# Kernel optimization log

Measured on AMD Instinct MI355X. Metric: run time of the kernel, lower is better.

The kernel has to match this reference:

```python
import jax, jax.numpy as jnp
import numpy as np

B, S, DIM = 128, 256, 512          # batch, grid tokens (16*16), input feature dim
D = 128                             # embedding_dim
K = 16384                           # num_embeddings
GH = GW = 16                        # grid size
EPS = 1e-12


def setup_inputs() -> dict:
    key = jax.random.key(0)
    ks = jax.random.split(key, 10)
    return {
        "input_data_first": jax.random.normal(ks[0], (B, S, DIM), jnp.float32),
        "input_data_last": jax.random.normal(ks[1], (B, S, DIM), jnp.float32),
        "random_vector": jax.random.normal(ks[2], (B * 64, D), jnp.float32),
        "codebooks": jax.random.normal(ks[3], (K, D), jnp.float32),
        "W_in": jax.random.normal(ks[4], (DIM, D), jnp.float32) / np.sqrt(DIM),
        "b_in": jnp.zeros((D,), jnp.float32),
        "conv_w": jax.random.normal(ks[5], (D, D, 3, 3), jnp.float32) / np.sqrt(D * 9),
        "conv_b": jnp.zeros((D,), jnp.float32),
        "W_out": jax.random.normal(ks[6], (D, DIM), jnp.float32) / np.sqrt(D),
        "b_out": jnp.zeros((DIM,), jnp.float32),
        "codebooks_used": jnp.zeros((K,), jnp.int32),
    }


def _encode(x, W_in, b_in, conv_w, conv_b):
    h = x @ W_in + b_in                                  # [B,S,D]
    h = jnp.transpose(h, (0, 2, 1)).reshape(B, D, GH, GW)  # [B,D,16,16]
    h = jax.lax.conv_general_dilated(
        h, conv_w, window_strides=(2, 2), padding=[(1, 1), (1, 1)],
        dimension_numbers=("NCHW", "OIHW", "NCHW"))
    h = h + conv_b[None, :, None, None]                  # [B,D,8,8]
    h = h.reshape(B, D, -1)                              # [B,D,64]
    h = jnp.transpose(h, (0, 2, 1)).reshape(-1, D)       # [B*64, D]
    return h


def reference(input_data_first, input_data_last, random_vector, codebooks,
              W_in, b_in, conv_w, conv_b, W_out, b_out, codebooks_used):
    e_first = _encode(input_data_first, W_in, b_in, conv_w, conv_b)
    e_last = _encode(input_data_last, W_in, b_in, conv_w, conv_b)
    x = e_last - e_first                                 # [N,D]

    # squared-distance to every codebook entry: [N,K]
    dists = (jnp.sum(x * x, axis=1, keepdims=True)
             - 2.0 * (x @ codebooks.T)
             + jnp.sum(codebooks * codebooks, axis=1)[None, :])
    min_indices = jnp.argmin(dists, axis=1)              # [N]
    hard_q = codebooks[min_indices]                      # [N,D]

    norm_res = jnp.sqrt(jnp.sum((x - hard_q) ** 2, axis=1, keepdims=True))
    norm_rnd = jnp.sqrt(jnp.sum(random_vector ** 2, axis=1, keepdims=True))
    vq_error = (norm_res / norm_rnd + EPS) * random_vector
    quantized = x + vq_error                             # [N,D]

    counts = jnp.zeros((K,), jnp.float32).at[min_indices].add(1.0)
    avg_probs = counts / x.shape[0]
    perplexity = jnp.exp(-jnp.sum(avg_probs * jnp.log(avg_probs + EPS)))

    new_used = codebooks_used + counts.astype(jnp.int32)

    # decode (faithful to torch: raw memory reinterpretation, not inverse transpose)
    q = quantized.reshape(B, D, -1)                      # [B,D,64]
    q = jnp.transpose(q, (0, 2, 1))                      # [B,64,D]
    out = q @ W_out + b_out                              # [B,64,DIM]
    return out, perplexity, new_used, min_indices.reshape(B, -1)
```

## Files before the change

### kernel.cpp

```cpp
#include <hip/hip_runtime.h>
#include <math.h>

#define NROWS 8192
#define KCB   16384

using frag_ab = __attribute__((ext_vector_type(8))) short;
using frag_cd = __attribute__((ext_vector_type(4))) float;
using f32x4   = __attribute__((ext_vector_type(4))) float;

__device__ inline unsigned short f2bf(float f) {
    unsigned u = __float_as_uint(f);
    return (unsigned short)((u + 0x7FFFu + ((u >> 16) & 1u)) >> 16);
}

__global__ __launch_bounds__(256) void k_wt(const float* __restrict__ cw,
                                            float* __restrict__ W2) {
    int gid = blockIdx.x * 256 + threadIdx.x;
    if (gid >= 147456) return;
    int co = gid & 127;
    int ci = (gid >> 7) & 127;
    int kk = gid >> 14;
    W2[gid] = cw[(size_t)co * 1152 + ci * 9 + kk];
}

__global__ __launch_bounds__(256) void k_c2(const float* __restrict__ cb,
                                            float* __restrict__ c2f) {
    int k = blockIdx.x * 256 + threadIdx.x;
    const float* row = cb + (size_t)k * 128;
    double s = 0.0;
    #pragma unroll
    for (int d = 0; d < 128; d += 4) {
        float4 v = *(const float4*)(row + d);
        s += (double)v.x * v.x + (double)v.y * v.y
           + (double)v.z * v.z + (double)v.w * v.w;
    }
    c2f[k] = (float)s + 1024.0f;
}

__global__ __launch_bounds__(256) void k_cbbf(const float* __restrict__ cb,
                                              unsigned short* __restrict__ Cbb) {
    int gid = blockIdx.x * 256 + threadIdx.x;
    float4 v = ((const float4*)cb)[gid];
    ushort4 o;
    o.x = f2bf(v.x); o.y = f2bf(v.y); o.z = f2bf(v.z); o.w = f2bf(v.w);
    ((ushort4*)Cbb)[gid] = o;
}

__global__ __launch_bounds__(256) void k_encode_gemm(
    const float* __restrict__ last, const float* __restrict__ first,
    const float* __restrict__ W_in, double* __restrict__ H)
{
    __shared__ double As[32][64];
    __shared__ float  Bs[32][128];
    const int tid  = threadIdx.x;
    const int row0 = blockIdx.x * 64;
    const int tx = tid & 31;
    const int ty = tid >> 5;

    double acc[8][4];
    #pragma unroll
    for (int r = 0; r < 8; ++r)
        #pragma unroll
        for (int j = 0; j < 4; ++j) acc[r][j] = 0.0;

    for (int d0 = 0; d0 < 512; d0 += 32) {
        #pragma unroll
        for (int it = 0; it < 2; ++it) {
            int flat = it * 1024 + tid * 4;
            int r = flat >> 5, d = flat & 31;
            const float4 l4 = *(const float4*)(last  + (size_t)(row0 + r) * 512 + d0 + d);
            const float4 f4 = *(const float4*)(first + (size_t)(row0 + r) * 512 + d0 + d);
            As[d + 0][r] = (double)l4.x - (double)f4.x;
            As[d + 1][r] = (double)l4.y - (double)f4.y;
            As[d + 2][r] = (double)l4.z - (double)f4.z;
            As[d + 3][r] = (double)l4.w - (double)f4.w;
        }
        #pragma unroll
        for (int it = 0; it < 4; ++it) {
            int flat = it * 1024 + tid * 4;
            int d = flat >> 7, c = flat & 127;
            *(float4*)&Bs[d][c] = *(const float4*)(W_in + (size_t)(d0 + d) * 128 + c);
        }
        __syncthreads();
        #pragma unroll 4
        for (int d = 0; d < 32; ++d) {
            double a[8];
            #pragma unroll
            for (int q = 0; q < 4; ++q) {
                double2 t = *(const double2*)&As[d][ty * 8 + 2 * q];
                a[2 * q] = t.x; a[2 * q + 1] = t.y;
            }
            float4 bf = *(const float4*)&Bs[d][tx * 4];
            double b[4] = {(double)bf.x, (double)bf.y, (double)bf.z, (double)bf.w};
            #pragma unroll
            for (int r = 0; r < 8; ++r)
                #pragma unroll
                for (int j = 0; j < 4; ++j)
                    acc[r][j] = fma(a[r], b[j], acc[r][j]);
        }
        __syncthreads();
    }
    #pragma unroll
    for (int r = 0; r < 8; ++r) {
        double* o = H + (size_t)(row0 + ty * 8 + r) * 128 + tx * 4;
        o[0] = acc[r][0]; o[1] = acc[r][1]; o[2] = acc[r][2]; o[3] = acc[r][3];
    }
}

__global__ __launch_bounds__(256) void k_conv(
    const double* __restrict__ H, const float* __restrict__ W2,
    double* __restrict__ X, unsigned short* __restrict__ Xb)
{
    __shared__ double Hs[3 * 16 * 128];
    const int b   = blockIdx.x >> 3;
    const int oh  = blockIdx.x & 7;
    const int tid = threadIdx.x;
    const int ih0 = 2 * oh - 1;
    for (int it = 0; it < 24; ++it) {
        int idx = it * 256 + tid;
        int r = idx >> 11;
        int rem = idx & 2047;
        int ih = ih0 + r;
        Hs[idx] = (ih >= 0) ? H[(size_t)b * 32768 + (size_t)ih * 2048 + rem] : 0.0;
    }
    __syncthreads();
    const int co   = tid & 127;
    const int half = tid >> 7;
    const int iwb  = half * 8 - 1;
    double acc[4] = {0, 0, 0, 0};
    for (int ci = 0; ci < 128; ++ci) {
        #pragma unroll
        for (int kh = 0; kh < 3; ++kh) {
            double in[9];
            #pragma unroll
            for (int t = 0; t < 9; ++t) {
                int iw = iwb + t;
                in[t] = (iw >= 0) ? Hs[kh * 2048 + iw * 128 + ci] : 0.0;
            }
            #pragma unroll
            for (int kw = 0; kw < 3; ++kw) {
                double w = (double)W2[(size_t)((kh * 3 + kw) * 128 + ci) * 128 + co];
                #pragma unroll
                for (int i = 0; i < 4; ++i)
                    acc[i] = fma(in[2 * i + kw], w, acc[i]);
            }
        }
    }
    #pragma unroll
    for (int i = 0; i < 4; ++i) {
        int ow = half * 4 + i;
        size_t n = (size_t)b * 64 + oh * 8 + ow;
        X [n * 128 + co] = acc[i];
        Xb[n * 128 + co] = f2bf((float)acc[i]);
    }
}

__global__ __launch_bounds__(256) void k_dist_mfma(
    const unsigned short* __restrict__ Xb, const unsigned short* __restrict__ Cbb,
    const float* __restrict__ c2f, int* __restrict__ cand)
{
    __shared__ __align__(16) unsigned short Xs[128 * 128];
    __shared__ __align__(16) unsigned short Cs[128 * 128];
    const int tid   = threadIdx.x;
    const int row0  = blockIdx.x * 128;
    const int split = blockIdx.y;
    const int lane  = tid & 63;
    const int w     = tid >> 6;
    const int quad  = lane >> 4;
    const int lm    = lane & 15;
    const int cw    = (w & 1) * 64;
    const int rw    = (w >> 1) * 64;

    #pragma unroll
    for (int it = 0; it < 8; ++it) {
        int flat = it * 256 + tid;
        int r = flat >> 4, ch = flat & 15;
        *(uint4*)&Xs[r * 128 + (((ch ^ r) & 15) << 3) + (ch & 16 ? 0 : 0)] =
            *(const uint4*)(Xb + (size_t)(row0 + r) * 128 + ch * 8);
    }

    unsigned k1[4], k2[4];
    #pragma unroll
    for (int j = 0; j < 4; ++j) { k1[j] = 0xFFFFFFFFu; k2[j] = 0xFFFFFFFFu; }

    for (int chunk = 0; chunk < 16; ++chunk) {
        const int kb = split * 2048 + chunk * 128;
        if (chunk) __syncthreads();
        #pragma unroll
        for (int it = 0; it < 8; ++it) {
            int flat = it * 256 + tid;
            int r = flat >> 4, ch = flat & 15;
            *(uint4*)&Cs[r * 128 + ((ch ^ (r & 15)) << 3)] =
                *(const uint4*)(Cbb + (size_t)(kb + r) * 128 + ch * 8);
        }
        __syncthreads();

        frag_cd acc[4][4];
        #pragma unroll
        for (int i = 0; i < 4; ++i)
            #pragma unroll
            for (int j = 0; j < 4; ++j)
                #pragma unroll
                for (int r = 0; r < 4; ++r) acc[i][j][r] = 0.f;

        #pragma unroll
        for (int kk = 0; kk < 4; ++kk) {
            const int chs = ((kk * 4 + quad) ^ lm) << 3;
            frag_ab a[4], b[4];
            #pragma unroll
            for (int i = 0; i < 4; ++i)
                a[i] = *(const frag_ab*)&Cs[(cw + i * 16 + lm) * 128 + chs];
            #pragma unroll
            for (int j = 0; j < 4; ++j)
                b[j] = *(const frag_ab*)&Xs[(rw + j * 16 + lm) * 128 + chs];
            #pragma unroll
            for (int i = 0; i < 4; ++i)
                #pragma unroll
                for (int j = 0; j < 4; ++j)
                    acc[i][j] = __builtin_amdgcn_mfma_f32_16x16x32_bf16(
                        a[i], b[j], acc[i][j], 0, 0, 0);
        }

        const int ib = chunk * 128 + cw + quad * 4;
        #pragma unroll
        for (int i = 0; i < 4; ++i) {
            f32x4 c2v = *(const f32x4*)(c2f + kb + cw + i * 16 + quad * 4);
            #pragma unroll
            for (int j = 0; j < 4; ++j) {
                #pragma unroll
                for (int r = 0; r < 4; ++r) {
                    float u = fmaf(-2.f, acc[i][j][r], c2v[r]);
                    unsigned key = (__float_as_uint(u) & 0xFFFFF800u)
                                 | (unsigned)(ib + i * 16 + r);
                    unsigned nk1 = min(key, k1[j]);
                    k2[j] = min(max(key, k1[j]), k2[j]);
                    k1[j] = nk1;
                }
            }
        }
    }

    __syncthreads();
    uint2* kred = (uint2*)Cs;
    #pragma unroll
    for (int j = 0; j < 4; ++j)
        kred[(rw + j * 16 + lm) * 8 + (w & 1) * 4 + quad] = make_uint2(k1[j], k2[j]);
    __syncthreads();
    if (tid < 128) {
        unsigned b1 = 0xFFFFFFFFu, b2 = 0xFFFFFFFFu;
        for (int e = 0; e < 8; ++e) {
            uint2 kv = kred[tid * 8 + e];
            unsigned n1 = min(kv.x, b1); b2 = min(max(kv.x, b1), b2); b1 = n1;
            n1 = min(kv.y, b1);          b2 = min(max(kv.y, b1), b2); b1 = n1;
        }
        int base = split * 2048;
        int* o = cand + (size_t)(row0 + tid) * 16 + split * 2;
        o[0] = base + (int)(b1 & 0x7FFu);
        o[1] = base + (int)(b2 & 0x7FFu);
    }
}

__global__ __launch_bounds__(256) void k_refine(
    const double* __restrict__ X, const float* __restrict__ cb,
    const int* __restrict__ cand, const float* __restrict__ rnd,
    int* __restrict__ counts, float* __restrict__ quant,
    float* __restrict__ out_mi)
{
    const int wid  = threadIdx.x >> 6;
    const int lane = threadIdx.x & 63;
    const int row  = blockIdx.x * 4 + wid;
    const double x0 = X[(size_t)row * 128 + lane];
    const double x1 = X[(size_t)row * 128 + 64 + lane];
    double bestv = 1e300; int bestk = 0;
    for (int c = 0; c < 16; ++c) {
        int k = cand[(size_t)row * 16 + c] & (KCB - 1);
        double t0 = x0 - (double)cb[(size_t)k * 128 + lane];
        double t1 = x1 - (double)cb[(size_t)k * 128 + 64 + lane];
        double s = t0 * t0 + t1 * t1;
        #pragma unroll
        for (int off = 32; off > 0; off >>= 1) s += __shfl_xor(s, off, 64);
        if (s < bestv) { bestv = s; bestk = k; }
    }
    double r0 = (double)rnd[(size_t)row * 128 + lane];
    double r1 = (double)rnd[(size_t)row * 128 + 64 + lane];
    double rs = r0 * r0 + r1 * r1;
    #pragma unroll
    for (int off = 32; off > 0; off >>= 1) rs += __shfl_xor(rs, off, 64);
    double ratio = sqrt(bestv) / sqrt(rs) + 1e-12;
    quant[(size_t)row * 128 + lane]      = (float)(x0 + ratio * r0);
    quant[(size_t)row * 128 + 64 + lane] = (float)(x1 + ratio * r1);
    if (lane == 0) {
        out_mi[row] = (float)bestk;
        atomicAdd(counts + bestk, 1);
    }
}

__global__ __launch_bounds__(256) void k_perplex(
    const int* __restrict__ counts, const int* __restrict__ used_in,
    float* __restrict__ out_used, float* __restrict__ out_perp)
{
    __shared__ double red[256];
    int tid = threadIdx.x;
    double e = 0.0;
    for (int k = tid; k < KCB; k += 256) {
        int c = counts[k];
        out_used[k] = (float)(used_in[k] + c);
        if (c > 0) {
            double p = (double)c / 8192.0;
            e += p * log(p + 1e-12);
        }
    }
    red[tid] = e;
    __syncthreads();
    for (int s = 128; s > 0; s >>= 1) {
        if (tid < s) red[tid] += red[tid + s];
        __syncthreads();
    }
    if (tid == 0) out_perp[0] = (float)exp(-red[0]);
}

__global__ __launch_bounds__(256) void k_decode(
    const float* __restrict__ quant, const float* __restrict__ W_out,
    const float* __restrict__ b_out, float* __restrict__ out)
{
    __shared__ float As[8192];
    __shared__ float Bs[8192];
    const int tid = threadIdx.x;
    const int m0  = blockIdx.x * 64;
    const int b   = blockIdx.y;
    #pragma unroll
    for (int it = 0; it < 8; ++it) {
        int flat = it * 1024 + tid * 4;
        *(float4*)&As[flat] = *(const float4*)(quant + (size_t)b * 8192 + flat);
        int d2 = flat >> 6, m = flat & 63;
        *(float4*)&Bs[flat] = *(const float4*)(W_out + (size_t)d2 * 512 + m0 + m);
    }
    __syncthreads();
    const int tx = tid & 15, ty = tid >> 4;
    float acc[4][4];
    #pragma unroll
    for (int i = 0; i < 4; ++i)
        #pragma unroll
        for (int j = 0; j < 4; ++j) acc[i][j] = 0.f;
    #pragma unroll 8
    for (int d2 = 0; d2 < 128; ++d2) {
        float4 a  = *(const float4*)&As[d2 * 64 + ty * 4];
        float4 b4 = *(const float4*)&Bs[d2 * 64 + tx * 4];
        float av[4] = {a.x, a.y, a.z, a.w};
        float bv[4] = {b4.x, b4.y, b4.z, b4.w};
        #pragma unroll
        for (int i = 0; i < 4; ++i)
            #pragma unroll
            for (int j = 0; j < 4; ++j)
                acc[i][j] = fmaf(av[i], bv[j], acc[i][j]);
    }
    float4 bo = *(const float4*)(b_out + m0 + tx * 4);
    float bob[4] = {bo.x, bo.y, bo.z, bo.w};
    #pragma unroll
    for (int i = 0; i < 4; ++i) {
        int s2 = ty * 4 + i;
        float4 o;
        o.x = acc[i][0] + bob[0];
        o.y = acc[i][1] + bob[1];
        o.z = acc[i][2] + bob[2];
        o.w = acc[i][3] + bob[3];
        *(float4*)(out + (size_t)b * 32768 + (size_t)s2 * 512 + m0 + tx * 4) = o;
    }
}

extern "C" void kernel_launch(void* const* d_in, const int* in_sizes, int n_in,
                              void* d_out, int out_size, void* d_ws, size_t ws_size,
                              hipStream_t stream) {
    const float* first  = (const float*)d_in[0];
    const float* last   = (const float*)d_in[1];
    const float* rnd    = (const float*)d_in[2];
    const float* cb     = (const float*)d_in[3];
    const float* W_in   = (const float*)d_in[4];
    const float* conv_w = (const float*)d_in[6];
    const float* W_out  = (const float*)d_in[8];
    const float* b_out  = (const float*)d_in[9];
    const int*   used   = (const int*)d_in[10];

    float* out      = (float*)d_out;
    float* out_perp = out + 4194304;
    float* out_used = out + 4194305;
    float* out_mi   = out + 4194305 + 16384;

    char* ws = (char*)d_ws;
    double*         H      = (double*)(ws);
    double*         X      = (double*)(ws + 33554432);
    unsigned short* Cbb    = (unsigned short*)(ws + 41943040);
    float*          W2     = (float*) (ws + 46137344);
    float*          c2f    = (float*) (ws + 46727168);
    int*            cand   = (int*)   (ws + 46792704);
    float*          quant  = (float*) (ws + 47316992);
    int*            counts = (int*)   (ws + 51511296);
    unsigned short* Xb     = (unsigned short*)(ws + 51576832);

    hipMemsetAsync(counts, 0, KCB * sizeof(int), stream);
    k_wt<<<576, 256, 0, stream>>>(conv_w, W2);
    k_c2<<<64, 256, 0, stream>>>(cb, c2f);
    k_cbbf<<<2048, 256, 0, stream>>>(cb, Cbb);
    k_encode_gemm<<<512, 256, 0, stream>>>(last, first, W_in, H);
    k_conv<<<1024, 256, 0, stream>>>(H, W2, X, Xb);
    k_dist_mfma<<<dim3(64, 8), 256, 0, stream>>>(Xb, Cbb, c2f, cand);
    k_refine<<<2048, 256, 0, stream>>>(X, cb, cand, rnd, counts, quant, out_mi);
    k_perplex<<<1, 256, 0, stream>>>(counts, used, out_used, out_perp);
    k_decode<<<dim3(8, 128), 256, 0, stream>>>(quant, W_out, b_out, out);
}
```

Baseline: 530.9 us.

## Retile fp64 encode GEMM with double-buffered smem and optional split-K

Replaces the encode GEMM with a 128x128 tile kernel that computes 8x8 fp64 outputs per thread and double-buffers shared memory, prefetching the next K slice into registers while the current one is computed. When the workspace is large enough, it splits K across two grid slices that write separate partial H buffers, and the conv kernel sums them when it loads. The aim is more arithmetic per shared-memory read, fewer sync stalls, and enough blocks to fill the device. The cost is higher register pressure and, under split-K, an extra 32MB partial buffer to write and read back.

```diff
diff --git a/kernel.cpp b/kernel.cpp
--- a/kernel.cpp
+++ b/kernel.cpp
@@ -46,69 +46,112 @@
     ((ushort4*)Cbb)[gid] = o;
 }
 
-__global__ __launch_bounds__(256) void k_encode_gemm(
+__global__ __launch_bounds__(256, 2) void k_enc2(
     const float* __restrict__ last, const float* __restrict__ first,
-    const float* __restrict__ W_in, double* __restrict__ H)
-{
-    __shared__ double As[32][64];
-    __shared__ float  Bs[32][128];
+    const float* __restrict__ W_in, double* __restrict__ Hp0,
+    double* __restrict__ Hp1, int ksteps)
+{
+    __shared__ double As[2][16][128];
+    __shared__ float  Bs[2][16][2][64];
     const int tid  = threadIdx.x;
-    const int row0 = blockIdx.x * 64;
-    const int tx = tid & 31;
-    const int ty = tid >> 5;
-
-    double acc[8][4];
+    const int row0 = blockIdx.x * 128;
+    const int kb0  = blockIdx.y * ksteps * 16;
+    const int tx = tid & 15;
+    const int ty = tid >> 4;
+    double* Hout = blockIdx.y ? Hp1 : Hp0;
+
+    const int ar[2] = { (tid * 4) >> 4, (1024 + tid * 4) >> 4 };
+    const int ad[2] = { (tid * 4) & 15, (1024 + tid * 4) & 15 };
+    const int bd[2] = { (tid * 4) >> 7, (1024 + tid * 4) >> 7 };
+    const int bc[2] = { (tid * 4) & 127, (1024 + tid * 4) & 127 };
+
+    double acc[8][8];
     #pragma unroll
     for (int r = 0; r < 8; ++r)
         #pragma unroll
-        for (int j = 0; j < 4; ++j) acc[r][j] = 0.0;
-
-    for (int d0 = 0; d0 < 512; d0 += 32) {
-        #pragma unroll
-        for (int it = 0; it < 2; ++it) {
-            int flat = it * 1024 + tid * 4;
-            int r = flat >> 5, d = flat & 31;
-            const float4 l4 = *(const float4*)(last  + (size_t)(row0 + r) * 512 + d0 + d);
-            const float4 f4 = *(const float4*)(first + (size_t)(row0 + r) * 512 + d0 + d);
-            As[d + 0][r] = (double)l4.x - (double)f4.x;
-            As[d + 1][r] = (double)l4.y - (double)f4.y;
-            As[d + 2][r] = (double)l4.z - (double)f4.z;
-            As[d + 3][r] = (double)l4.w - (double)f4.w;
-        }
-        #pragma unroll
-        for (int it = 0; it < 4; ++it) {
-            int flat = it * 1024 + tid * 4;
-            int d = flat >> 7, c = flat & 127;
-            *(float4*)&Bs[d][c] = *(const float4*)(W_in + (size_t)(d0 + d) * 128 + c);
-        }
-        __syncthreads();
-        #pragma unroll 4
-        for (int d = 0; d < 32; ++d) {
+        for (int j = 0; j < 8; ++j) acc[r][j] = 0.0;
+
+    float4 l4[2], f4[2], w4[2];
+
+    #pragma unroll
+    for (int it = 0; it < 2; ++it) {
+        l4[it] = *(const float4*)(last  + (size_t)(row0 + ar[it]) * 512 + kb0 + ad[it]);
+        f4[it] = *(const float4*)(first + (size_t)(row0 + ar[it]) * 512 + kb0 + ad[it]);
+        w4[it] = *(const float4*)(W_in  + (size_t)(kb0 + bd[it]) * 128 + bc[it]);
+    }
+    #pragma unroll
+    for (int it = 0; it < 2; ++it) {
+        As[0][ad[it] + 0][ar[it]] = (double)l4[it].x - (double)f4[it].x;
+        As[0][ad[it] + 1][ar[it]] = (double)l4[it].y - (double)f4[it].y;
+        As[0][ad[it] + 2][ar[it]] = (double)l4[it].z - (double)f4[it].z;
+        As[0][ad[it] + 3][ar[it]] = (double)l4[it].w - (double)f4[it].w;
+        int h = (bc[it] >> 2) & 1, ib = (bc[it] >> 3) * 4;
+        *(float4*)&Bs[0][bd[it]][h][ib] = w4[it];
+    }
+    __syncthreads();
+
+    for (int t = 0; t < ksteps; ++t) {
+        const int buf = t & 1;
+        if (t + 1 < ksteps) {
+            const int kb = kb0 + (t + 1) * 16;
+            #pragma unroll
+            for (int it = 0; it < 2; ++it) {
+                l4[it] = *(const float4*)(last  + (size_t)(row0 + ar[it]) * 512 + kb + ad[it]);
+                f4[it] = *(const float4*)(first + (size_t)(row0 + ar[it]) * 512 + kb + ad[it]);
+                w4[it] = *(const float4*)(W_in  + (size_t)(kb + bd[it]) * 128 + bc[it]);
+            }
+        }
+
+        const double (*Asb)[128] = As[buf];
+        const float  (*Bsb)[2][64] = Bs[buf];
+        #pragma unroll
+        for (int d = 0; d < 16; ++d) {
             double a[8];
             #pragma unroll
             for (int q = 0; q < 4; ++q) {
-                double2 t = *(const double2*)&As[d][ty * 8 + 2 * q];
-                a[2 * q] = t.x; a[2 * q + 1] = t.y;
-            }
-            float4 bf = *(const float4*)&Bs[d][tx * 4];
-            double b[4] = {(double)bf.x, (double)bf.y, (double)bf.z, (double)bf.w};
+                double2 t2 = *(const double2*)&Asb[d][ty * 8 + 2 * q];
+                a[2 * q] = t2.x; a[2 * q + 1] = t2.y;
+            }
+            float4 b0 = *(const float4*)&Bsb[d][0][tx * 4];
+            float4 b1 = *(const float4*)&Bsb[d][1][tx * 4];
+            double b[8] = {(double)b0.x, (double)b0.y, (double)b0.z, (double)b0.w,
+                           (double)b1.x, (double)b1.y, (double)b1.z, (double)b1.w};
             #pragma unroll
             for (int r = 0; r < 8; ++r)
                 #pragma unroll
-                for (int j = 0; j < 4; ++j)
+                for (int j = 0; j < 8; ++j)
                     acc[r][j] = fma(a[r], b[j], acc[r][j]);
         }
+
+        if (t + 1 < ksteps) {
+            const int nb = buf ^ 1;
+            #pragma unroll
+            for (int it = 0; it < 2; ++it) {
+                As[nb][ad[it] + 0][ar[it]] = (double)l4[it].x - (double)f4[it].x;
+                As[nb][ad[it] + 1][ar[it]] = (double)l4[it].y - (double)f4[it].y;
+                As[nb][ad[it] + 2][ar[it]] = (double)l4[it].z - (double)f4[it].z;
+                As[nb][ad[it] + 3][ar[it]] = (double)l4[it].w - (double)f4[it].w;
+                int h = (bc[it] >> 2) & 1, ib = (bc[it] >> 3) * 4;
+                *(float4*)&Bs[nb][bd[it]][h][ib] = w4[it];
+            }
+        }
         __syncthreads();
     }
+
     #pragma unroll
     for (int r = 0; r < 8; ++r) {
-        double* o = H + (size_t)(row0 + ty * 8 + r) * 128 + tx * 4;
-        o[0] = acc[r][0]; o[1] = acc[r][1]; o[2] = acc[r][2]; o[3] = acc[r][3];
+        double* o = Hout + (size_t)(row0 + ty * 8 + r) * 128 + tx * 8;
+        #pragma unroll
+        for (int q = 0; q < 4; ++q) {
+            double2 t2; t2.x = acc[r][2 * q]; t2.y = acc[r][2 * q + 1];
+            *(double2*)(o + 2 * q) = t2;
+        }
     }
 }
 
 __global__ __launch_bounds__(256) void k_conv(
-    const double* __restrict__ H, const float* __restrict__ W2,
+    const double* __restrict__ H0, const double* __restrict__ H1, int nsplit,
+    const float* __restrict__ W2,
     double* __restrict__ X, unsigned short* __restrict__ Xb)
 {
     __shared__ double Hs[3 * 16 * 128];
@@ -121,7 +164,13 @@
         int r = idx >> 11;
         int rem = idx & 2047;
         int ih = ih0 + r;
-        Hs[idx] = (ih >= 0) ? H[(size_t)b * 32768 + (size_t)ih * 2048 + rem] : 0.0;
+        double v = 0.0;
+        if (ih >= 0) {
+            size_t g = (size_t)b * 32768 + (size_t)ih * 2048 + rem;
+            v = H0[g];
+            if (nsplit == 2) v += H1[g];
+        }
+        Hs[idx] = v;
     }
     __syncthreads();
     const int co   = tid & 127;
@@ -396,13 +445,17 @@
     float*          quant  = (float*) (ws + 47316992);
     int*            counts = (int*)   (ws + 51511296);
     unsigned short* Xb     = (unsigned short*)(ws + 51576832);
+    double*         H1     = (double*)(ws + 53673984);
+
+    const int nsplit = (ws_size >= 87228416ull) ? 2 : 1;
+    const int ksteps = 32 / nsplit;
 
     hipMemsetAsync(counts, 0, KCB * sizeof(int), stream);
     k_wt<<<576, 256, 0, stream>>>(conv_w, W2);
     k_c2<<<64, 256, 0, stream>>>(cb, c2f);
     k_cbbf<<<2048, 256, 0, stream>>>(cb, Cbb);
-    k_encode_gemm<<<512, 256, 0, stream>>>(last, first, W_in, H);
-    k_conv<<<1024, 256, 0, stream>>>(H, W2, X, Xb);
+    k_enc2<<<dim3(256, nsplit), 256, 0, stream>>>(last, first, W_in, H, H1, ksteps);
+    k_conv<<<1024, 256, 0, stream>>>(H, H1, nsplit, W2, X, Xb);
     k_dist_mfma<<<dim3(64, 8), 256, 0, stream>>>(Xb, Cbb, c2f, cand);
     k_refine<<<2048, 256, 0, stream>>>(X, cb, cand, rnd, counts, quant, out_mi);
     k_perplex<<<1, 256, 0, stream>>>(counts, used, out_used, out_perp);
```

After: 1.461 ms. 2.75x slower.
